# Kernel tuning notes

Hardware: AMD Instinct MI355X
Metric: run time of the kernel (lower is better)

The kernel has to match this reference:

```python
import jax, jax.numpy as jnp
import numpy as np

B, S, L = 8, 64, 6          # graphs, spatial side, orientation layers
K = 6                       # Chebyshev order
IN_D, HID, OUT_D = 3, 128, 10


def _grid_edges(num_graphs, s, l):
    b, o, y, x = np.meshgrid(np.arange(num_graphs), np.arange(l), np.arange(s), np.arange(s), indexing='ij')
    nid = ((b * l + o) * s + y) * s + x  # linear node id, [B,L,s,s]
    srcs, dsts = [], []
    def add(a, c):
        srcs.append(a.ravel()); dsts.append(c.ravel())
    add(nid[..., :-1], nid[..., 1:]); add(nid[..., 1:], nid[..., :-1])                 # x-neighbors
    add(nid[:, :, :-1, :], nid[:, :, 1:, :]); add(nid[:, :, 1:, :], nid[:, :, :-1, :])  # y-neighbors
    nxt = np.roll(nid, -1, axis=1)                                                     # orientation ring
    add(nid, nxt); add(nxt, nid)
    return np.stack([np.concatenate(srcs), np.concatenate(dsts)]).astype(np.int32)


def _cluster_spatial(num_graphs, s, l):
    b, o, y, x = np.meshgrid(np.arange(num_graphs), np.arange(l), np.arange(s), np.arange(s), indexing='ij')
    h = s // 2
    return (((b * l + o) * h + y // 2) * h + x // 2).ravel().astype(np.int32)


def setup_inputs() -> dict:
    key = jax.random.key(0)
    ks = jax.random.split(key, 20)
    inp = {}
    N1 = B * L * S * S
    inp['x'] = jax.random.normal(ks[0], (N1, IN_D), jnp.float32)
    for i, s in enumerate([S, S // 2, S // 4]):
        ei = _grid_edges(B, s, L)
        inp[f'edge_index{i+1}'] = jnp.asarray(ei)
        inp[f'edge_attr{i+1}'] = jax.random.uniform(ks[1 + i], (ei.shape[1],), jnp.float32, 0.1, 1.0)
    inp['cluster1'] = jnp.asarray(_cluster_spatial(B, S, L))
    inp['cluster2'] = jnp.asarray(_cluster_spatial(B, S // 2, L))
    inp['cluster3'] = jnp.asarray(_cluster_spatial(B, S // 4, L))
    s4 = S // 8
    b, o, y, x = np.meshgrid(np.arange(B), np.arange(L), np.arange(s4), np.arange(s4), indexing='ij')
    inp['cluster4'] = jnp.asarray(((b * s4 + y) * s4 + x).ravel().astype(np.int32))  # collapse orientation axis
    inp['batch_final'] = jnp.asarray(np.repeat(np.arange(B), s4 * s4).astype(np.int32))
    dims = [(IN_D, HID), (HID, HID), (HID, HID), (HID, HID), (HID, HID), (HID, OUT_D)]
    for i, (di, do) in enumerate(dims):
        inp[f'W{i+1}'] = jax.random.normal(ks[8 + i], (K, di, do), jnp.float32) / np.float32(np.sqrt(di * K))
        inp[f'b{i+1}'] = jnp.zeros((do,), jnp.float32)
    for i in range(5):
        inp[f'gamma{i+1}'] = jnp.ones((HID,), jnp.float32)
        inp[f'beta{i+1}'] = jnp.zeros((HID,), jnp.float32)
    return inp


def _cheb_conv(x, ei, ea, W, b):
    # Chebyshev polynomial graph conv: out = sum_k T_k(L) x @ W_k + b,
    # with T0=x, T1=Lx, Tk = 2 L T_{k-1} - T_{k-2}; L applied via edge gather/scatter.
    src, dst = ei[0], ei[1]
    n = x.shape[0]
    def lap(v):
        return jax.ops.segment_sum(ea[:, None] * v[src], dst, num_segments=n)
    Tx0 = x
    out = Tx0 @ W[0]
    Tx1 = lap(x)
    out = out + Tx1 @ W[1]
    for k in range(2, W.shape[0]):
        Tx2 = 2.0 * lap(Tx1) - Tx0
        out = out + Tx2 @ W[k]
        Tx0, Tx1 = Tx1, Tx2
    return out + b


def _bn(x, g, bt):
    # BatchNorm1d in training mode (batch statistics, biased variance, eps=1e-5)
    mu = x.mean(0)
    var = x.var(0)
    return g * (x - mu) * jax.lax.rsqrt(var + 1e-5) + bt


def reference(x, edge_index1, edge_attr1, edge_index2, edge_attr2, edge_index3, edge_attr3, cluster1, cluster2, cluster3, cluster4, batch_final, W1, b1, W2, b2, W3, b3, W4, b4, W5, b5, W6, b6, gamma1, beta1, gamma2, beta2, gamma3, beta3, gamma4, beta4, gamma5, beta5):
    h = jax.nn.relu(_bn(_cheb_conv(x, edge_index1, edge_attr1, W1, b1), gamma1, beta1))
    h = jax.nn.relu(_bn(_cheb_conv(h, edge_index1, edge_attr1, W2, b2), gamma2, beta2))
    h = jax.ops.segment_max(h, cluster1, num_segments=B * L * (S // 2) ** 2)
    h = jax.nn.relu(_bn(_cheb_conv(h, edge_index2, edge_attr2, W3, b3), gamma3, beta3))
    h = jax.nn.relu(_bn(_cheb_conv(h, edge_index2, edge_attr2, W4, b4), gamma4, beta4))
    h = jax.ops.segment_max(h, cluster2, num_segments=B * L * (S // 4) ** 2)
    h = jax.nn.relu(_bn(_cheb_conv(h, edge_index3, edge_attr3, W5, b5), gamma5, beta5))
    h = jax.nn.relu(_cheb_conv(h, edge_index3, edge_attr3, W6, b6))
    h = jax.ops.segment_max(h, cluster3, num_segments=B * L * (S // 8) ** 2)   # spatial pool 3
    h = jax.ops.segment_max(h, cluster4, num_segments=B * (S // 8) ** 2)        # orientation pool
    g = jax.ops.segment_max(h, batch_final, num_segments=B)                     # global max pool
    return jax.nn.log_softmax(g, axis=1)
```

## Files before the change

kernel.cpp:

```cpp
#include <hip/hip_runtime.h>
#include <math.h>

#define L_OR 6
#define N_BL 48

typedef unsigned short u16;
typedef __attribute__((ext_vector_type(8))) short s8v;
typedef __attribute__((ext_vector_type(4))) float f4v;

#define N1 196608
#define N2 49152
#define N3 12288

__device__ u16   g_cat[(size_t)N1 * 768 + 1024];
__device__ u16   g_O[(size_t)N1 * 128];
__device__ float g_Tt[5 * (size_t)N1 * 3];
__device__ u16   g_Bt[128 * 768 + 4096];
__device__ u16   g_W6t[16 * 768];
__device__ float g_O10[(size_t)N3 * 10];
__device__ float g_p3[3072 * 10];
__device__ float g_p4[512 * 10];
__device__ float g_part[1536 * 256];
__device__ float g_part2[64 * 256];
__device__ float g_mean[128];
__device__ float g_inv[128];

__device__ __forceinline__ float b2f(u16 v) {
    return __uint_as_float(((unsigned)v) << 16);
}
__device__ __forceinline__ u16 f2b(float f) {
    unsigned u = __float_as_uint(f);
    return (u16)((u + 0x7FFFu + ((u >> 16) & 1u)) >> 16);
}

template<int S>
__global__ __launch_bounds__(256)
void lap128b(u16* __restrict__ cat, int outSlot, int inSlot, int tppSlot,
             const float* __restrict__ ea, float alpha)
{
    int node = blockIdx.x * 16 + (threadIdx.x >> 4);
    int c8   = threadIdx.x & 15;

    const int x = node % S;
    const int y = (node / S) % S;
    const int g = node / (S * S);
    const int o = g % L_OR;
    const int b = g / L_OR;
    const int szx = N_BL * S * (S - 1);

    float a[8] = {0.f, 0.f, 0.f, 0.f, 0.f, 0.f, 0.f, 0.f};
    const int chOff = inSlot * 128 + c8 * 8;

    auto gather = [&](int src, float w) {
        s8v v = *(const s8v*)(cat + (size_t)src * 768 + chOff);
#pragma unroll
        for (int j = 0; j < 8; ++j) a[j] += w * b2f((u16)v[j]);
    };

    const int basex = (g * S + y) * (S - 1);
    if (x > 0)     gather(node - 1, ea[basex + x - 1]);
    if (x < S - 1) gather(node + 1, ea[szx + basex + x]);
    if (y > 0)     gather(node - S, ea[2 * szx + (g * (S - 1) + y - 1) * S + x]);
    if (y < S - 1) gather(node + S, ea[3 * szx + (g * (S - 1) + y) * S + x]);
    {   int op = (o == 0) ? L_OR - 1 : o - 1;
        int sp = ((b * L_OR + op) * S + y) * S + x;
        gather(sp, ea[4 * szx + sp]);
    }
    {   int on = (o == L_OR - 1) ? 0 : o + 1;
        int sn = ((b * L_OR + on) * S + y) * S + x;
        gather(sn, ea[4 * szx + N_BL * S * S + node]);
    }

    float r[8];
#pragma unroll
    for (int j = 0; j < 8; ++j) r[j] = alpha * a[j];
    if (tppSlot >= 0) {
        s8v t = *(const s8v*)(cat + (size_t)node * 768 + tppSlot * 128 + c8 * 8);
#pragma unroll
        for (int j = 0; j < 8; ++j) r[j] -= b2f((u16)t[j]);
    }
    s8v ov;
#pragma unroll
    for (int j = 0; j < 8; ++j) ov[j] = (short)f2b(r[j]);
    *(s8v*)(cat + (size_t)node * 768 + outSlot * 128 + c8 * 8) = ov;
}

template<int S>
__global__ __launch_bounds__(256)
void lap3_kernel(float* __restrict__ out, const float* __restrict__ in,
                 const float* __restrict__ tpp, const float* __restrict__ ea,
                 float alpha)
{
    const int NN = N_BL * S * S;
    int n = blockIdx.x * 256 + threadIdx.x;
    if (n >= NN) return;
    const int x = n % S, y = (n / S) % S, g = n / (S * S);
    const int o = g % L_OR, b = g / L_OR;
    const int szx = N_BL * S * (S - 1);

    float a0 = 0.f, a1 = 0.f, a2 = 0.f;
    auto gather = [&](int src, float w) {
        a0 += w * in[src * 3 + 0];
        a1 += w * in[src * 3 + 1];
        a2 += w * in[src * 3 + 2];
    };
    const int basex = (g * S + y) * (S - 1);
    if (x > 0)     gather(n - 1, ea[basex + x - 1]);
    if (x < S - 1) gather(n + 1, ea[szx + basex + x]);
    if (y > 0)     gather(n - S, ea[2 * szx + (g * (S - 1) + y - 1) * S + x]);
    if (y < S - 1) gather(n + S, ea[3 * szx + (g * (S - 1) + y) * S + x]);
    { int op = (o == 0) ? L_OR - 1 : o - 1; int sp = ((b * L_OR + op) * S + y) * S + x;
      gather(sp, ea[4 * szx + sp]); }
    { int on = (o == L_OR - 1) ? 0 : o + 1; int sn = ((b * L_OR + on) * S + y) * S + x;
      gather(sn, ea[4 * szx + N_BL * S * S + n]); }

    float r0 = alpha * a0, r1 = alpha * a1, r2 = alpha * a2;
    if (tpp) { r0 -= tpp[n * 3 + 0]; r1 -= tpp[n * 3 + 1]; r2 -= tpp[n * 3 + 2]; }
    out[n * 3 + 0] = r0; out[n * 3 + 1] = r1; out[n * 3 + 2] = r2;
}

__global__ __launch_bounds__(256)
void gemm_mfma_cat(u16* __restrict__ O, const u16* __restrict__ A,
                   const u16* __restrict__ Bf, const float* __restrict__ bias,
                   float* __restrict__ partials)
{
    __shared__ u16 Bs[2][4096];
    const int tid  = threadIdx.x;
    const int wave = tid >> 6;
    const int lane = tid & 63;
    const int lrow = lane & 15;
    const int kg   = lane >> 4;
    const int r0   = blockIdx.x * 128 + wave * 32;

    const u16* A0 = A + (size_t)(r0 + lrow) * 768 + kg * 8;
    const u16* A1 = A0 + (size_t)16 * 768;

    f4v acc[2][8] = {};

    {
        s8v s0 = *(const s8v*)(Bf + tid * 8);
        s8v s1 = *(const s8v*)(Bf + 2048 + tid * 8);
        *(s8v*)&Bs[0][tid * 8] = s0;
        *(s8v*)&Bs[0][2048 + tid * 8] = s1;
    }
    s8v a0 = *(const s8v*)(A0);
    s8v a1 = *(const s8v*)(A1);
    __syncthreads();

#pragma unroll 1
    for (int p = 0; p < 24; ++p) {
        const int cur = p & 1, nxt = cur ^ 1;
        const u16* src = Bf + (p + 1) * 4096;
        s8v nb0 = *(const s8v*)(src + tid * 8);
        s8v nb1 = *(const s8v*)(src + 2048 + tid * 8);
        s8v a0n = *(const s8v*)(A0 + (p + 1) * 32);
        s8v a1n = *(const s8v*)(A1 + (p + 1) * 32);
#pragma unroll
        for (int ct = 0; ct < 8; ++ct) {
            s8v b = *(const s8v*)&Bs[cur][(ct * 64 + lane) * 8];
            acc[0][ct] = __builtin_amdgcn_mfma_f32_16x16x32_bf16(a0, b, acc[0][ct], 0, 0, 0);
            acc[1][ct] = __builtin_amdgcn_mfma_f32_16x16x32_bf16(a1, b, acc[1][ct], 0, 0, 0);
        }
        __syncthreads();
        *(s8v*)&Bs[nxt][tid * 8] = nb0;
        *(s8v*)&Bs[nxt][2048 + tid * 8] = nb1;
        __syncthreads();
        a0 = a0n; a1 = a1n;
    }

    __shared__ float sred[4][2][8][16];
    float cs[8], cq[8];
#pragma unroll
    for (int ct = 0; ct < 8; ++ct) { cs[ct] = 0.f; cq[ct] = 0.f; }

#pragma unroll
    for (int s = 0; s < 2; ++s)
#pragma unroll
        for (int ct = 0; ct < 8; ++ct) {
            int col = ct * 16 + lrow;
            float bv = bias[col];
#pragma unroll
            for (int j = 0; j < 4; ++j) {
                int row = r0 + s * 16 + kg * 4 + j;
                float v = acc[s][ct][j] + bv;
                O[(size_t)row * 128 + col] = f2b(v);
                cs[ct] += v; cq[ct] += v * v;
            }
        }
#pragma unroll
    for (int ct = 0; ct < 8; ++ct) {
        cs[ct] += __shfl_xor(cs[ct], 16); cs[ct] += __shfl_xor(cs[ct], 32);
        cq[ct] += __shfl_xor(cq[ct], 16); cq[ct] += __shfl_xor(cq[ct], 32);
    }
    if (lane < 16) {
#pragma unroll
        for (int ct = 0; ct < 8; ++ct) {
            sred[wave][0][ct][lane] = cs[ct];
            sred[wave][1][ct][lane] = cq[ct];
        }
    }
    __syncthreads();
    if (threadIdx.x < 128) {
        int ct = threadIdx.x >> 4, lr = threadIdx.x & 15;
        float S = 0.f, Q = 0.f;
#pragma unroll
        for (int w = 0; w < 4; ++w) { S += sred[w][0][ct][lr]; Q += sred[w][1][ct][lr]; }
        partials[blockIdx.x * 256 + threadIdx.x]       = S;
        partials[blockIdx.x * 256 + 128 + threadIdx.x] = Q;
    }
}

__global__ __launch_bounds__(256)
void wprep(const float* __restrict__ W, u16* __restrict__ Bf, int base)
{
    int idx = blockIdx.x * 256 + threadIdx.x;
    int j    = idx & 7;
    int lane = (idx >> 3) & 63;
    int ct   = (idx >> 9) & 7;
    int k0s  = idx >> 12;
    int k    = k0s * 32 + (lane >> 4) * 8 + j;
    int col  = ct * 16 + (lane & 15);
    int slot = k >> 7, d = k & 127;
    int wk = slot - base; if (wk < 0) wk += 6;
    Bf[idx] = f2b(W[(size_t)wk * 16384 + d * 128 + col]);
}

__global__ __launch_bounds__(256)
void w6prep(const float* __restrict__ W, u16* __restrict__ W6t, int base)
{
    int idx = blockIdx.x * 256 + threadIdx.x;
    if (idx >= 16 * 768) return;
    int c = idx / 768, kk = idx % 768;
    int slot = kk >> 7, d = kk & 127;
    int wk = slot - base; if (wk < 0) wk += 6;
    W6t[idx] = (c < 10) ? f2b(W[(size_t)wk * 1280 + d * 10 + c]) : (u16)0;
}

__global__ __launch_bounds__(256)
void l1gemm(u16* __restrict__ O, const float* __restrict__ T0,
            const float* __restrict__ Tt, const float* __restrict__ W,
            const float* __restrict__ bias, float* __restrict__ partials)
{
    __shared__ float Ts[128][18];
    __shared__ float sh[2][128], sh2[2][128];
    int tid = threadIdx.x;
    int rbase = blockIdx.x * 128;
    for (int i = tid; i < 128 * 18; i += 256) {
        int r = i / 18, t = i % 18;
        int k = t / 3, j = t % 3;
        Ts[r][t] = (k == 0) ? T0[(size_t)(rbase + r) * 3 + j]
                            : Tt[(size_t)(k - 1) * N1 * 3 + (size_t)(rbase + r) * 3 + j];
    }
    __syncthreads();
    int c = tid & 127, h = tid >> 7;
    float w[18];
#pragma unroll
    for (int k = 0; k < 6; ++k)
#pragma unroll
        for (int j = 0; j < 3; ++j) w[k * 3 + j] = W[(size_t)k * 384 + j * 128 + c];
    float bv = bias[c];
    float S = 0.f, Q = 0.f;
    for (int i = 0; i < 64; ++i) {
        int r = h * 64 + i;
        float acc = bv;
#pragma unroll
        for (int t = 0; t < 18; ++t) acc += Ts[r][t] * w[t];
        O[(size_t)(rbase + r) * 128 + c] = f2b(acc);
        S += acc; Q += acc * acc;
    }
    sh[h][c] = S; sh2[h][c] = Q;
    __syncthreads();
    if (tid < 128) {
        partials[blockIdx.x * 256 + tid]       = sh[0][tid] + sh[1][tid];
        partials[blockIdx.x * 256 + 128 + tid] = sh2[0][tid] + sh2[1][tid];
    }
}

__global__ __launch_bounds__(256)
void out10_cat(float* __restrict__ O10, const u16* __restrict__ cat,
               const u16* __restrict__ W6t, const float* __restrict__ bias)
{
    int col = threadIdx.x & 15;
    int row = blockIdx.x * 16 + (threadIdx.x >> 4);
    const u16* a = cat + (size_t)row * 768;
    const u16* w = W6t + (size_t)col * 768;
    float acc = 0.f;
#pragma unroll 4
    for (int k0 = 0; k0 < 768; k0 += 8) {
        s8v av = *(const s8v*)(a + k0);
        s8v wv = *(const s8v*)(w + k0);
#pragma unroll
        for (int j = 0; j < 8; ++j)
            acc += b2f((u16)av[j]) * b2f((u16)wv[j]);
    }
    if (col < 10)
        O10[(size_t)row * 10 + col] = fmaxf(acc + bias[col], 0.f);
}

__global__ __launch_bounds__(256)
void bn_reduce1(const float* __restrict__ partials, int nblk,
                float* __restrict__ part2)
{
    int tid = threadIdx.x;
    float S = 0.f;
#pragma unroll 4
    for (int b = blockIdx.x; b < nblk; b += 64)
        S += partials[(size_t)b * 256 + tid];
    part2[blockIdx.x * 256 + tid] = S;
}

__global__ __launch_bounds__(256)
void bn_finalize2(const float* __restrict__ part2, int N,
                  float* __restrict__ meanb, float* __restrict__ invstd)
{
    int tid = threadIdx.x;
    int c = tid & 127, h = tid >> 7;
    float S = 0.f, Q = 0.f;
#pragma unroll 8
    for (int b = h; b < 64; b += 2) {
        S += part2[b * 256 + c];
        Q += part2[b * 256 + 128 + c];
    }
    __shared__ float shS[2][128], shQ[2][128];
    shS[h][c] = S; shQ[h][c] = Q;
    __syncthreads();
    if (tid < 128) {
        float Sa = shS[0][tid] + shS[1][tid];
        float Qa = shQ[0][tid] + shQ[1][tid];
        float inv_n = 1.f / (float)N;
        float mu = Sa * inv_n;
        float var = Qa * inv_n - mu * mu;
        meanb[tid] = mu;
        invstd[tid] = rsqrtf(var + 1e-5f);
    }
}

__global__ __launch_bounds__(256)
void bn_apply_cat8(const u16* __restrict__ O, u16* __restrict__ cat, int slot,
                   const float* __restrict__ meanb, const float* __restrict__ invstd,
                   const float* __restrict__ g, const float* __restrict__ bt)
{
    int idx = blockIdx.x * 256 + threadIdx.x;
    int c8 = idx & 15;
    size_t row = idx >> 4;
    s8v v = *(const s8v*)(O + row * 128 + c8 * 8);
    s8v ov;
#pragma unroll
    for (int j = 0; j < 8; ++j) {
        int c = c8 * 8 + j;
        float val = (b2f((u16)v[j]) - meanb[c]) * invstd[c] * g[c] + bt[c];
        ov[j] = (short)f2b(fmaxf(val, 0.f));
    }
    *(s8v*)(cat + row * 768 + slot * 128 + c8 * 8) = ov;
}

__global__ __launch_bounds__(256)
void bn_apply_pool8(const u16* __restrict__ O, u16* __restrict__ cat, int outSlot,
                    int s, int Nout,
                    const float* __restrict__ meanb, const float* __restrict__ invstd,
                    const float* __restrict__ g, const float* __restrict__ bt)
{
    int idx = blockIdx.x * 256 + threadIdx.x;
    if (idx >= Nout * 16) return;
    int c8 = idx & 15;
    int n2 = idx >> 4;
    int h  = s >> 1;
    int x2 = n2 % h;
    int y2 = (n2 / h) % h;
    int gg = n2 / (h * h);
    int base = (gg * s + 2 * y2) * s + 2 * x2;
    s8v v0 = *(const s8v*)(O + (size_t)base * 128 + c8 * 8);
    s8v v1 = *(const s8v*)(O + (size_t)(base + 1) * 128 + c8 * 8);
    s8v v2 = *(const s8v*)(O + (size_t)(base + s) * 128 + c8 * 8);
    s8v v3 = *(const s8v*)(O + (size_t)(base + s + 1) * 128 + c8 * 8);
    s8v ov;
#pragma unroll
    for (int j = 0; j < 8; ++j) {
        int c = c8 * 8 + j;
        float sc = invstd[c] * g[c];
        float so = bt[c] - meanb[c] * sc;
        float m =          b2f((u16)v0[j]) * sc + so;
        m = fmaxf(m, b2f((u16)v1[j]) * sc + so);
        m = fmaxf(m, b2f((u16)v2[j]) * sc + so);
        m = fmaxf(m, b2f((u16)v3[j]) * sc + so);
        ov[j] = (short)f2b(fmaxf(m, 0.f));
    }
    *(s8v*)(cat + (size_t)n2 * 768 + outSlot * 128 + c8 * 8) = ov;
}

__global__ __launch_bounds__(256)
void pool_spatial(float* __restrict__ out, const float* __restrict__ in,
                  int s, int D, int Nout)
{
    int idx = blockIdx.x * 256 + threadIdx.x;
    if (idx >= Nout * D) return;
    int c  = idx % D;
    int n2 = idx / D;
    int h  = s >> 1;
    int x2 = n2 % h;
    int y2 = (n2 / h) % h;
    int g  = n2 / (h * h);
    int base = (g * s + 2 * y2) * s + 2 * x2;
    float m = in[(size_t)base * D + c];
    m = fmaxf(m, in[(size_t)(base + 1) * D + c]);
    m = fmaxf(m, in[(size_t)(base + s) * D + c]);
    m = fmaxf(m, in[(size_t)(base + s + 1) * D + c]);
    out[(size_t)n2 * D + c] = m;
}

__global__ __launch_bounds__(256)
void pool_orient(float* __restrict__ out, const float* __restrict__ in)
{
    int idx = blockIdx.x * 256 + threadIdx.x;
    if (idx >= 512 * 10) return;
    int c = idx % 10;
    int n = idx / 10;
    int x = n % 8, y = (n / 8) % 8, b = n / 64;
    float m = -INFINITY;
    for (int o = 0; o < L_OR; ++o)
        m = fmaxf(m, in[(size_t)((((b * L_OR + o) * 8 + y) * 8 + x)) * 10 + c]);
    out[idx] = m;
}

__global__ __launch_bounds__(128)
void global_pool_logsoftmax(const float* __restrict__ in, float* __restrict__ out)
{
    __shared__ float G[8][10];
    __shared__ float rowm[8], rowl[8];
    int t = threadIdx.x;
    if (t < 80) {
        int b = t / 10, c = t % 10;
        float m = -INFINITY;
        for (int p = 0; p < 64; ++p)
            m = fmaxf(m, in[(size_t)(b * 64 + p) * 10 + c]);
        G[b][c] = m;
    }
    __syncthreads();
    if (t < 8) {
        float m = -INFINITY;
        for (int c = 0; c < 10; ++c) m = fmaxf(m, G[t][c]);
        float s = 0.f;
        for (int c = 0; c < 10; ++c) s += expf(G[t][c] - m);
        rowm[t] = m; rowl[t] = logf(s);
    }
    __syncthreads();
    if (t < 80) {
        int b = t / 10, c = t % 10;
        out[t] = G[b][c] - rowm[b] - rowl[b];
    }
}

static void launch_lapb(u16* cat, int os, int is, int ts, const float* ea,
                        int S, int N, float alpha, hipStream_t st)
{
    dim3 grid(N / 16), block(256);
    if (S == 64)      hipLaunchKernelGGL(lap128b<64>, grid, block, 0, st, cat, os, is, ts, ea, alpha);
    else if (S == 32) hipLaunchKernelGGL(lap128b<32>, grid, block, 0, st, cat, os, is, ts, ea, alpha);
    else              hipLaunchKernelGGL(lap128b<16>, grid, block, 0, st, cat, os, is, ts, ea, alpha);
}

static void cheb_laps(u16* cat, int base, const float* ea, int S, int N, hipStream_t st)
{
    for (int k = 1; k < 6; ++k) {
        int os = (k + base) % 6;
        int is = (k - 1 + base) % 6;
        int ts = (k >= 2) ? (k - 2 + base) % 6 : -1;
        launch_lapb(cat, os, is, ts, ea, S, N, (k == 1) ? 1.f : 2.f, st);
    }
}

static void bn_reduce(float* part, float* part2, int nblk, int N,
                      float* meanb, float* invstd, hipStream_t st)
{
    hipLaunchKernelGGL(bn_reduce1, dim3(64), dim3(256), 0, st, part, nblk, part2);
    hipLaunchKernelGGL(bn_finalize2, dim3(1), dim3(256), 0, st, part2, N, meanb, invstd);
}

extern "C" void kernel_launch(void* const* d_in, const int* in_sizes, int n_in,
                              void* d_out, int out_size, void* d_ws, size_t ws_size,
                              hipStream_t stream)
{
    const float* x   = (const float*)d_in[0];
    const float* ea1 = (const float*)d_in[2];
    const float* ea2 = (const float*)d_in[4];
    const float* ea3 = (const float*)d_in[6];
    const float* W1  = (const float*)d_in[12];
    const float* b1  = (const float*)d_in[13];
    const float* W2  = (const float*)d_in[14];
    const float* b2  = (const float*)d_in[15];
    const float* W3  = (const float*)d_in[16];
    const float* b3  = (const float*)d_in[17];
    const float* W4  = (const float*)d_in[18];
    const float* b4  = (const float*)d_in[19];
    const float* W5  = (const float*)d_in[20];
    const float* b5  = (const float*)d_in[21];
    const float* W6  = (const float*)d_in[22];
    const float* b6  = (const float*)d_in[23];
    const float* g1  = (const float*)d_in[24];
    const float* be1 = (const float*)d_in[25];
    const float* g2  = (const float*)d_in[26];
    const float* be2 = (const float*)d_in[27];
    const float* g3  = (const float*)d_in[28];
    const float* be3 = (const float*)d_in[29];
    const float* g4  = (const float*)d_in[30];
    const float* be4 = (const float*)d_in[31];
    const float* g5  = (const float*)d_in[32];
    const float* be5 = (const float*)d_in[33];

    u16 *cat, *O, *Bt, *W6t;
    float *Tt, *O10, *p3, *p4, *part, *part2, *meanb, *invstd;
    if (hipGetSymbolAddress((void**)&cat, HIP_SYMBOL(g_cat)) != hipSuccess) return;
    if (hipGetSymbolAddress((void**)&O,   HIP_SYMBOL(g_O))   != hipSuccess) return;
    if (hipGetSymbolAddress((void**)&Tt,  HIP_SYMBOL(g_Tt))  != hipSuccess) return;
    if (hipGetSymbolAddress((void**)&Bt,  HIP_SYMBOL(g_Bt))  != hipSuccess) return;
    if (hipGetSymbolAddress((void**)&W6t, HIP_SYMBOL(g_W6t)) != hipSuccess) return;
    if (hipGetSymbolAddress((void**)&O10, HIP_SYMBOL(g_O10)) != hipSuccess) return;
    if (hipGetSymbolAddress((void**)&p3,  HIP_SYMBOL(g_p3))  != hipSuccess) return;
    if (hipGetSymbolAddress((void**)&p4,  HIP_SYMBOL(g_p4))  != hipSuccess) return;
    if (hipGetSymbolAddress((void**)&part,   HIP_SYMBOL(g_part))  != hipSuccess) return;
    if (hipGetSymbolAddress((void**)&part2,  HIP_SYMBOL(g_part2)) != hipSuccess) return;
    if (hipGetSymbolAddress((void**)&meanb,  HIP_SYMBOL(g_mean))  != hipSuccess) return;
    if (hipGetSymbolAddress((void**)&invstd, HIP_SYMBOL(g_inv))   != hipSuccess) return;

    dim3 blk(256);

    {
        float* t1 = Tt;
        float* t2 = Tt + (size_t)N1 * 3;
        float* t3 = Tt + (size_t)2 * N1 * 3;
        float* t4 = Tt + (size_t)3 * N1 * 3;
        float* t5 = Tt + (size_t)4 * N1 * 3;
        dim3 gl((N1 + 255) / 256);
        hipLaunchKernelGGL(lap3_kernel<64>, gl, blk, 0, stream, t1, x,  (const float*)nullptr, ea1, 1.f);
        hipLaunchKernelGGL(lap3_kernel<64>, gl, blk, 0, stream, t2, t1, x,  ea1, 2.f);
        hipLaunchKernelGGL(lap3_kernel<64>, gl, blk, 0, stream, t3, t2, t1, ea1, 2.f);
        hipLaunchKernelGGL(lap3_kernel<64>, gl, blk, 0, stream, t4, t3, t2, ea1, 2.f);
        hipLaunchKernelGGL(lap3_kernel<64>, gl, blk, 0, stream, t5, t4, t3, ea1, 2.f);
        hipLaunchKernelGGL(l1gemm, dim3(N1 / 128), blk, 0, stream, O, x, Tt, W1, b1, part);
    }
    bn_reduce(part, part2, N1 / 128, N1, meanb, invstd, stream);
    hipLaunchKernelGGL(bn_apply_cat8, dim3(N1 / 16), blk, 0, stream,
                       O, cat, 0, meanb, invstd, g1, be1);

    hipLaunchKernelGGL(wprep, dim3(384), blk, 0, stream, W2, Bt, 0);
    cheb_laps(cat, 0, ea1, 64, N1, stream);
    hipLaunchKernelGGL(gemm_mfma_cat, dim3(N1 / 128), blk, 0, stream, O, cat, Bt, b2, part);
    bn_reduce(part, part2, N1 / 128, N1, meanb, invstd, stream);
    hipLaunchKernelGGL(bn_apply_pool8, dim3(N2 / 16), blk, 0, stream,
                       O, cat, 5, 64, N2, meanb, invstd, g2, be2);

    hipLaunchKernelGGL(wprep, dim3(384), blk, 0, stream, W3, Bt, 5);
    cheb_laps(cat, 5, ea2, 32, N2, stream);
    hipLaunchKernelGGL(gemm_mfma_cat, dim3(N2 / 128), blk, 0, stream, O, cat, Bt, b3, part);
    bn_reduce(part, part2, N2 / 128, N2, meanb, invstd, stream);
    hipLaunchKernelGGL(bn_apply_cat8, dim3(N2 / 16), blk, 0, stream,
                       O, cat, 0, meanb, invstd, g3, be3);

    hipLaunchKernelGGL(wprep, dim3(384), blk, 0, stream, W4, Bt, 0);
    cheb_laps(cat, 0, ea2, 32, N2, stream);
    hipLaunchKernelGGL(gemm_mfma_cat, dim3(N2 / 128), blk, 0, stream, O, cat, Bt, b4, part);
    bn_reduce(part, part2, N2 / 128, N2, meanb, invstd, stream);
    hipLaunchKernelGGL(bn_apply_pool8, dim3(N3 / 16), blk, 0, stream,
                       O, cat, 5, 32, N3, meanb, invstd, g4, be4);

    hipLaunchKernelGGL(wprep, dim3(384), blk, 0, stream, W5, Bt, 5);
    cheb_laps(cat, 5, ea3, 16, N3, stream);
    hipLaunchKernelGGL(gemm_mfma_cat, dim3(N3 / 128), blk, 0, stream, O, cat, Bt, b5, part);
    bn_reduce(part, part2, N3 / 128, N3, meanb, invstd, stream);
    hipLaunchKernelGGL(bn_apply_cat8, dim3(N3 / 16), blk, 0, stream,
                       O, cat, 0, meanb, invstd, g5, be5);

    hipLaunchKernelGGL(w6prep, dim3(48), blk, 0, stream, W6, W6t, 0);
    cheb_laps(cat, 0, ea3, 16, N3, stream);
    hipLaunchKernelGGL(out10_cat, dim3(N3 / 16), blk, 0, stream, O10, cat, W6t, b6);

    hipLaunchKernelGGL(pool_spatial, dim3((3072 * 10 + 255) / 256), blk, 0, stream,
                       p3, O10, 16, 10, 3072);
    hipLaunchKernelGGL(pool_orient, dim3((512 * 10 + 255) / 256), blk, 0, stream, p4, p3);
    hipLaunchKernelGGL(global_pool_logsoftmax, dim3(1), dim3(128), 0, stream,
                       p4, (float*)d_out);
}
```

Measured before the change: 836.3 us.

## Precompute per-node edge weight tables and double GEMM K-step per stage

Adds an eaprep kernel that packs each node's six neighbour weights, with zeros at boundaries, plus orientation offsets into a contiguous 8-float table. The Laplacian kernels then read two float4s and gather without index arithmetic or branches. Boundary neighbours are clamped to valid nodes and weighted by zero, which adds some wasted loads. The lap kernel also uses packed bf16 conversion via inline asm, and the MFMA GEMM processes 64 K per stage with twice the shared memory, halving the barrier count.

```diff
diff --git a/kernel.cpp b/kernel.cpp
--- a/kernel.cpp
+++ b/kernel.cpp
@@ -15,8 +15,11 @@
 __device__ u16   g_cat[(size_t)N1 * 768 + 1024];
 __device__ u16   g_O[(size_t)N1 * 128];
 __device__ float g_Tt[5 * (size_t)N1 * 3];
-__device__ u16   g_Bt[128 * 768 + 4096];
+__device__ u16   g_Bt[128 * 768 + 8192];
 __device__ u16   g_W6t[16 * 768];
+__device__ float g_wt1[(size_t)N1 * 8];
+__device__ float g_wt2[(size_t)N2 * 8];
+__device__ float g_wt3[(size_t)N3 * 8];
 __device__ float g_O10[(size_t)N3 * 10];
 __device__ float g_p3[3072 * 10];
 __device__ float g_p4[512 * 10];
@@ -35,41 +38,63 @@
 
 template<int S>
 __global__ __launch_bounds__(256)
+void eaprep(float* __restrict__ wtab, const float* __restrict__ ea)
+{
+    const int NN = N_BL * S * S;
+    int n = blockIdx.x * 256 + threadIdx.x;
+    if (n >= NN) return;
+    int x = n % S, y = (n / S) % S, g = n / (S * S);
+    int o = g % L_OR, b = g / L_OR;
+    const int szx = N_BL * S * (S - 1);
+    const int basex = (g * S + y) * (S - 1);
+    float wxm = (x > 0)     ? ea[basex + x - 1] : 0.f;
+    float wxp = (x < S - 1) ? ea[szx + basex + x] : 0.f;
+    float wym = (y > 0)     ? ea[2 * szx + (g * (S - 1) + y - 1) * S + x] : 0.f;
+    float wyp = (y < S - 1) ? ea[3 * szx + (g * (S - 1) + y) * S + x] : 0.f;
+    int op_ = (o == 0) ? L_OR - 1 : o - 1;
+    int on_ = (o == L_OR - 1) ? 0 : o + 1;
+    int sp = ((b * L_OR + op_) * S + y) * S + x;
+    int sn = ((b * L_OR + on_) * S + y) * S + x;
+    float wom = ea[4 * szx + sp];
+    float wop = ea[4 * szx + N_BL * S * S + n];
+    float* w = wtab + (size_t)n * 8;
+    w[0] = wxm; w[1] = wxp; w[2] = wym; w[3] = wyp; w[4] = wom; w[5] = wop;
+    ((int*)w)[6] = sp - n;
+    ((int*)w)[7] = sn - n;
+}
+
+template<int S>
+__global__ __launch_bounds__(256)
 void lap128b(u16* __restrict__ cat, int outSlot, int inSlot, int tppSlot,
-             const float* __restrict__ ea, float alpha)
-{
+             const float* __restrict__ wtab, float alpha)
+{
+    const int NN = N_BL * S * S;
     int node = blockIdx.x * 16 + (threadIdx.x >> 4);
     int c8   = threadIdx.x & 15;
 
-    const int x = node % S;
-    const int y = (node / S) % S;
-    const int g = node / (S * S);
-    const int o = g % L_OR;
-    const int b = g / L_OR;
-    const int szx = N_BL * S * (S - 1);
-
+    float4 wa = *(const float4*)(wtab + (size_t)node * 8);
+    float4 wb = *(const float4*)(wtab + (size_t)node * 8 + 4);
+    int dsp = __float_as_int(wb.z);
+    int dsn = __float_as_int(wb.w);
+
+    int sxm = (node > 0)      ? node - 1 : 0;
+    int sxp = (node < NN - 1) ? node + 1 : node;
+    int sym = (node >= S)     ? node - S : node;
+    int syp = (node < NN - S) ? node + S : node;
+
+    const int chOff = inSlot * 128 + c8 * 8;
     float a[8] = {0.f, 0.f, 0.f, 0.f, 0.f, 0.f, 0.f, 0.f};
-    const int chOff = inSlot * 128 + c8 * 8;
-
     auto gather = [&](int src, float w) {
         s8v v = *(const s8v*)(cat + (size_t)src * 768 + chOff);
 #pragma unroll
         for (int j = 0; j < 8; ++j) a[j] += w * b2f((u16)v[j]);
     };
-
-    const int basex = (g * S + y) * (S - 1);
-    if (x > 0)     gather(node - 1, ea[basex + x - 1]);
-    if (x < S - 1) gather(node + 1, ea[szx + basex + x]);
-    if (y > 0)     gather(node - S, ea[2 * szx + (g * (S - 1) + y - 1) * S + x]);
-    if (y < S - 1) gather(node + S, ea[3 * szx + (g * (S - 1) + y) * S + x]);
-    {   int op = (o == 0) ? L_OR - 1 : o - 1;
-        int sp = ((b * L_OR + op) * S + y) * S + x;
-        gather(sp, ea[4 * szx + sp]);
-    }
-    {   int on = (o == L_OR - 1) ? 0 : o + 1;
-        int sn = ((b * L_OR + on) * S + y) * S + x;
-        gather(sn, ea[4 * szx + N_BL * S * S + node]);
-    }
+    gather(sxm, wa.x);
+    gather(sxp, wa.y);
+    gather(sym, wa.z);
+    gather(syp, wa.w);
+    gather(node + dsp, wb.x);
+    gather(node + dsn, wb.y);
 
     float r[8];
 #pragma unroll
@@ -79,24 +104,31 @@
 #pragma unroll
         for (int j = 0; j < 8; ++j) r[j] -= b2f((u16)t[j]);
     }
-    s8v ov;
-#pragma unroll
-    for (int j = 0; j < 8; ++j) ov[j] = (short)f2b(r[j]);
-    *(s8v*)(cat + (size_t)node * 768 + outSlot * 128 + c8 * 8) = ov;
+    uint4 ov;
+    asm("v_cvt_pk_bf16_f32 %0, %1, %2" : "=v"(ov.x) : "v"(r[0]), "v"(r[1]));
+    asm("v_cvt_pk_bf16_f32 %0, %1, %2" : "=v"(ov.y) : "v"(r[2]), "v"(r[3]));
+    asm("v_cvt_pk_bf16_f32 %0, %1, %2" : "=v"(ov.z) : "v"(r[4]), "v"(r[5]));
+    asm("v_cvt_pk_bf16_f32 %0, %1, %2" : "=v"(ov.w) : "v"(r[6]), "v"(r[7]));
+    *(uint4*)(cat + (size_t)node * 768 + outSlot * 128 + c8 * 8) = ov;
 }
 
 template<int S>
 __global__ __launch_bounds__(256)
 void lap3_kernel(float* __restrict__ out, const float* __restrict__ in,
-                 const float* __restrict__ tpp, const float* __restrict__ ea,
+                 const float* __restrict__ tpp, const float* __restrict__ wtab,
                  float alpha)
 {
     const int NN = N_BL * S * S;
     int n = blockIdx.x * 256 + threadIdx.x;
     if (n >= NN) return;
-    const int x = n % S, y = (n / S) % S, g = n / (S * S);
-    const int o = g % L_OR, b = g / L_OR;
-    const int szx = N_BL * S * (S - 1);
+    float4 wa = *(const float4*)(wtab + (size_t)n * 8);
+    float4 wb = *(const float4*)(wtab + (size_t)n * 8 + 4);
+    int dsp = __float_as_int(wb.z);
+    int dsn = __float_as_int(wb.w);
+    int sxm = (n > 0)      ? n - 1 : 0;
+    int sxp = (n < NN - 1) ? n + 1 : n;
+    int sym = (n >= S)     ? n - S : n;
+    int syp = (n < NN - S) ? n + S : n;
 
     float a0 = 0.f, a1 = 0.f, a2 = 0.f;
     auto gather = [&](int src, float w) {
@@ -104,15 +136,8 @@
         a1 += w * in[src * 3 + 1];
         a2 += w * in[src * 3 + 2];
     };
-    const int basex = (g * S + y) * (S - 1);
-    if (x > 0)     gather(n - 1, ea[basex + x - 1]);
-    if (x < S - 1) gather(n + 1, ea[szx + basex + x]);
-    if (y > 0)     gather(n - S, ea[2 * szx + (g * (S - 1) + y - 1) * S + x]);
-    if (y < S - 1) gather(n + S, ea[3 * szx + (g * (S - 1) + y) * S + x]);
-    { int op = (o == 0) ? L_OR - 1 : o - 1; int sp = ((b * L_OR + op) * S + y) * S + x;
-      gather(sp, ea[4 * szx + sp]); }
-    { int on = (o == L_OR - 1) ? 0 : o + 1; int sn = ((b * L_OR + on) * S + y) * S + x;
-      gather(sn, ea[4 * szx + N_BL * S * S + n]); }
+    gather(sxm, wa.x); gather(sxp, wa.y); gather(sym, wa.z); gather(syp, wa.w);
+    gather(n + dsp, wb.x); gather(n + dsn, wb.y);
 
     float r0 = alpha * a0, r1 = alpha * a1, r2 = alpha * a2;
     if (tpp) { r0 -= tpp[n * 3 + 0]; r1 -= tpp[n * 3 + 1]; r2 -= tpp[n * 3 + 2]; }
@@ -124,7 +149,7 @@
                    const u16* __restrict__ Bf, const float* __restrict__ bias,
                    float* __restrict__ partials)
 {
-    __shared__ u16 Bs[2][4096];
+    __shared__ u16 Bs[2][8192];
     const int tid  = threadIdx.x;
     const int wave = tid >> 6;
     const int lane = tid & 63;
@@ -137,35 +162,46 @@
 
     f4v acc[2][8] = {};
 
-    {
-        s8v s0 = *(const s8v*)(Bf + tid * 8);
-        s8v s1 = *(const s8v*)(Bf + 2048 + tid * 8);
-        *(s8v*)&Bs[0][tid * 8] = s0;
-        *(s8v*)&Bs[0][2048 + tid * 8] = s1;
-    }
-    s8v a0 = *(const s8v*)(A0);
-    s8v a1 = *(const s8v*)(A1);
+#pragma unroll
+    for (int i = 0; i < 4; ++i)
+        *(s8v*)&Bs[0][i * 2048 + tid * 8] = *(const s8v*)(Bf + i * 2048 + tid * 8);
+    s8v a00 = *(const s8v*)(A0);
+    s8v a10 = *(const s8v*)(A1);
+    s8v a01 = *(const s8v*)(A0 + 32);
+    s8v a11 = *(const s8v*)(A1 + 32);
     __syncthreads();
 
 #pragma unroll 1
-    for (int p = 0; p < 24; ++p) {
+    for (int p = 0; p < 12; ++p) {
         const int cur = p & 1, nxt = cur ^ 1;
-        const u16* src = Bf + (p + 1) * 4096;
+        const u16* src = Bf + (p + 1) * 8192;
         s8v nb0 = *(const s8v*)(src + tid * 8);
         s8v nb1 = *(const s8v*)(src + 2048 + tid * 8);
-        s8v a0n = *(const s8v*)(A0 + (p + 1) * 32);
-        s8v a1n = *(const s8v*)(A1 + (p + 1) * 32);
+        s8v nb2 = *(const s8v*)(src + 4096 + tid * 8);
+        s8v nb3 = *(const s8v*)(src + 6144 + tid * 8);
+        s8v na00 = *(const s8v*)(A0 + (p + 1) * 64);
+        s8v na10 = *(const s8v*)(A1 + (p + 1) * 64);
+        s8v na01 = *(const s8v*)(A0 + (p + 1) * 64 + 32);
+        s8v na11 = *(const s8v*)(A1 + (p + 1) * 64 + 32);
 #pragma unroll
         for (int ct = 0; ct < 8; ++ct) {
             s8v b = *(const s8v*)&Bs[cur][(ct * 64 + lane) * 8];
-            acc[0][ct] = __builtin_amdgcn_mfma_f32_16x16x32_bf16(a0, b, acc[0][ct], 0, 0, 0);
-            acc[1][ct] = __builtin_amdgcn_mfma_f32_16x16x32_bf16(a1, b, acc[1][ct], 0, 0, 0);
+            acc[0][ct] = __builtin_amdgcn_mfma_f32_16x16x32_bf16(a00, b, acc[0][ct], 0, 0, 0);
+            acc[1][ct] = __builtin_amdgcn_mfma_f32_16x16x32_bf16(a10, b, acc[1][ct], 0, 0, 0);
+        }
+#pragma unroll
+        for (int ct = 0; ct < 8; ++ct) {
+            s8v b = *(const s8v*)&Bs[cur][4096 + (ct * 64 + lane) * 8];
+            acc[0][ct] = __builtin_amdgcn_mfma_f32_16x16x32_bf16(a01, b, acc[0][ct], 0, 0, 0);
+            acc[1][ct] = __builtin_amdgcn_mfma_f32_16x16x32_bf16(a11, b, acc[1][ct], 0, 0, 0);
         }
         __syncthreads();
-        *(s8v*)&Bs[nxt][tid * 8] = nb0;
+        *(s8v*)&Bs[nxt][tid * 8]        = nb0;
         *(s8v*)&Bs[nxt][2048 + tid * 8] = nb1;
+        *(s8v*)&Bs[nxt][4096 + tid * 8] = nb2;
+        *(s8v*)&Bs[nxt][6144 + tid * 8] = nb3;
         __syncthreads();
-        a0 = a0n; a1 = a1n;
+        a00 = na00; a10 = na10; a01 = na01; a11 = na11;
     }
 
     __shared__ float sred[4][2][8][16];
@@ -450,22 +486,22 @@
     }
 }
 
-static void launch_lapb(u16* cat, int os, int is, int ts, const float* ea,
+static void launch_lapb(u16* cat, int os, int is, int ts, const float* wtab,
                         int S, int N, float alpha, hipStream_t st)
 {
     dim3 grid(N / 16), block(256);
-    if (S == 64)      hipLaunchKernelGGL(lap128b<64>, grid, block, 0, st, cat, os, is, ts, ea, alpha);
-    else if (S == 32) hipLaunchKernelGGL(lap128b<32>, grid, block, 0, st, cat, os, is, ts, ea, alpha);
-    else              hipLaunchKernelGGL(lap128b<16>, grid, block, 0, st, cat, os, is, ts, ea, alpha);
-}
-
-static void cheb_laps(u16* cat, int base, const float* ea, int S, int N, hipStream_t st)
+    if (S == 64)      hipLaunchKernelGGL(lap128b<64>, grid, block, 0, st, cat, os, is, ts, wtab, alpha);
+    else if (S == 32) hipLaunchKernelGGL(lap128b<32>, grid, block, 0, st, cat, os, is, ts, wtab, alpha);
+    else              hipLaunchKernelGGL(lap128b<16>, grid, block, 0, st, cat, os, is, ts, wtab, alpha);
+}
+
+static void cheb_laps(u16* cat, int base, const float* wtab, int S, int N, hipStream_t st)
 {
     for (int k = 1; k < 6; ++k) {
         int os = (k + base) % 6;
         int is = (k - 1 + base) % 6;
         int ts = (k >= 2) ? (k - 2 + base) % 6 : -1;
-        launch_lapb(cat, os, is, ts, ea, S, N, (k == 1) ? 1.f : 2.f, st);
+        launch_lapb(cat, os, is, ts, wtab, S, N, (k == 1) ? 1.f : 2.f, st);
     }
 }
 
@@ -508,7 +544,7 @@
     const float* be5 = (const float*)d_in[33];
 
     u16 *cat, *O, *Bt, *W6t;
-    float *Tt, *O10, *p3, *p4, *part, *part2, *meanb, *invstd;
+    float *Tt, *O10, *p3, *p4, *part, *part2, *meanb, *invstd, *wt1, *wt2, *wt3;
     if (hipGetSymbolAddress((void**)&cat, HIP_SYMBOL(g_cat)) != hipSuccess) return;
     if (hipGetSymbolAddress((void**)&O,   HIP_SYMBOL(g_O))   != hipSuccess) return;
     if (hipGetSymbolAddress((void**)&Tt,  HIP_SYMBOL(g_Tt))  != hipSuccess) return;
@@ -521,8 +557,15 @@
     if (hipGetSymbolAddress((void**)&part2,  HIP_SYMBOL(g_part2)) != hipSuccess) return;
     if (hipGetSymbolAddress((void**)&meanb,  HIP_SYMBOL(g_mean))  != hipSuccess) return;
     if (hipGetSymbolAddress((void**)&invstd, HIP_SYMBOL(g_inv))   != hipSuccess) return;
+    if (hipGetSymbolAddress((void**)&wt1, HIP_SYMBOL(g_wt1)) != hipSuccess) return;
+    if (hipGetSymbolAddress((void**)&wt2, HIP_SYMBOL(g_wt2)) != hipSuccess) return;
+    if (hipGetSymbolAddress((void**)&wt3, HIP_SYMBOL(g_wt3)) != hipSuccess) return;
 
     dim3 blk(256);
+
+    hipLaunchKernelGGL(eaprep<64>, dim3(N1 / 256), blk, 0, stream, wt1, ea1);
+    hipLaunchKernelGGL(eaprep<32>, dim3(N2 / 256), blk, 0, stream, wt2, ea2);
+    hipLaunchKernelGGL(eaprep<16>, dim3(N3 / 256), blk, 0, stream, wt3, ea3);
 
     {
         float* t1 = Tt;
@@ -531,11 +574,11 @@
         float* t4 = Tt + (size_t)3 * N1 * 3;
         float* t5 = Tt + (size_t)4 * N1 * 3;
         dim3 gl((N1 + 255) / 256);
-        hipLaunchKernelGGL(lap3_kernel<64>, gl, blk, 0, stream, t1, x,  (const float*)nullptr, ea1, 1.f);
-        hipLaunchKernelGGL(lap3_kernel<64>, gl, blk, 0, stream, t2, t1, x,  ea1, 2.f);
-        hipLaunchKernelGGL(lap3_kernel<64>, gl, blk, 0, stream, t3, t2, t1, ea1, 2.f);
-        hipLaunchKernelGGL(lap3_kernel<64>, gl, blk, 0, stream, t4, t3, t2, ea1, 2.f);
-        hipLaunchKernelGGL(lap3_kernel<64>, gl, blk, 0, stream, t5, t4, t3, ea1, 2.f);
+        hipLaunchKernelGGL(lap3_kernel<64>, gl, blk, 0, stream, t1, x,  (const float*)nullptr, wt1, 1.f);
+        hipLaunchKernelGGL(lap3_kernel<64>, gl, blk, 0, stream, t2, t1, x,  wt1, 2.f);
+        hipLaunchKernelGGL(lap3_kernel<64>, gl, blk, 0, stream, t3, t2, t1, wt1, 2.f);
+        hipLaunchKernelGGL(lap3_kernel<64>, gl, blk, 0, stream, t4, t3, t2, wt1, 2.f);
+        hipLaunchKernelGGL(lap3_kernel<64>, gl, blk, 0, stream, t5, t4, t3, wt1, 2.f);
         hipLaunchKernelGGL(l1gemm, dim3(N1 / 128), blk, 0, stream, O, x, Tt, W1, b1, part);
     }
     bn_reduce(part, part2, N1 / 128, N1, meanb, invstd, stream);
@@ -543,35 +586,35 @@
                        O, cat, 0, meanb, invstd, g1, be1);
 
     hipLaunchKernelGGL(wprep, dim3(384), blk, 0, stream, W2, Bt, 0);
-    cheb_laps(cat, 0, ea1, 64, N1, stream);
+    cheb_laps(cat, 0, wt1, 64, N1, stream);
     hipLaunchKernelGGL(gemm_mfma_cat, dim3(N1 / 128), blk, 0, stream, O, cat, Bt, b2, part);
     bn_reduce(part, part2, N1 / 128, N1, meanb, invstd, stream);
     hipLaunchKernelGGL(bn_apply_pool8, dim3(N2 / 16), blk, 0, stream,
                        O, cat, 5, 64, N2, meanb, invstd, g2, be2);
 
     hipLaunchKernelGGL(wprep, dim3(384), blk, 0, stream, W3, Bt, 5);
-    cheb_laps(cat, 5, ea2, 32, N2, stream);
+    cheb_laps(cat, 5, wt2, 32, N2, stream);
     hipLaunchKernelGGL(gemm_mfma_cat, dim3(N2 / 128), blk, 0, stream, O, cat, Bt, b3, part);
     bn_reduce(part, part2, N2 / 128, N2, meanb, invstd, stream);
     hipLaunchKernelGGL(bn_apply_cat8, dim3(N2 / 16), blk, 0, stream,
                        O, cat, 0, meanb, invstd, g3, be3);
 
     hipLaunchKernelGGL(wprep, dim3(384), blk, 0, stream, W4, Bt, 0);
-    cheb_laps(cat, 0, ea2, 32, N2, stream);
+    cheb_laps(cat, 0, wt2, 32, N2, stream);
     hipLaunchKernelGGL(gemm_mfma_cat, dim3(N2 / 128), blk, 0, stream, O, cat, Bt, b4, part);
     bn_reduce(part, part2, N2 / 128, N2, meanb, invstd, stream);
     hipLaunchKernelGGL(bn_apply_pool8, dim3(N3 / 16), blk, 0, stream,
                        O, cat, 5, 32, N3, meanb, invstd, g4, be4);
 
     hipLaunchKernelGGL(wprep, dim3(384), blk, 0, stream, W5, Bt, 5);
-    cheb_laps(cat, 5, ea3, 16, N3, stream);
+    cheb_laps(cat, 5, wt3, 16, N3, stream);
     hipLaunchKernelGGL(gemm_mfma_cat, dim3(N3 / 128), blk, 0, stream, O, cat, Bt, b5, part);
     bn_reduce(part, part2, N3 / 128, N3, meanb, invstd, stream);
     hipLaunchKernelGGL(bn_apply_cat8, dim3(N3 / 16), blk, 0, stream,
                        O, cat, 0, meanb, invstd, g5, be5);
 
     hipLaunchKernelGGL(w6prep, dim3(48), blk, 0, stream, W6, W6t, 0);
-    cheb_laps(cat, 0, ea3, 16, N3, stream);
+    cheb_laps(cat, 0, wt3, 16, N3, stream);
     hipLaunchKernelGGL(out10_cat, dim3(N3 / 16), blk, 0, stream, O10, cat, W6t, b6);
 
     hipLaunchKernelGGL(pool_spatial, dim3((3072 * 10 + 255) / 256), blk, 0, stream,
```

After: 795.1 us. 4.9% less time.
